# Kernel tuning notes

Measured on AMD Instinct MI355X. Metric: run time of the kernel, lower is better.

The kernel has to match this reference:

```python
import jax, jax.numpy as jnp
import numpy as np

B, T, D, H, F = 4, 1024, 1024, 16, 4096
DH = D // H
EPS = 1e-5


def _ln(x, g, b):
    m = jnp.mean(x, axis=-1, keepdims=True)
    v = jnp.mean((x - m) ** 2, axis=-1, keepdims=True)
    return (x - m) * jax.lax.rsqrt(v + EPS) * g + b


def setup_inputs() -> dict:
    key = jax.random.key(0)
    ks = jax.random.split(key, 16)
    w = lambda k, s: jax.random.normal(k, s, jnp.float32) * 0.02
    return {
        "x": jax.random.normal(ks[0], (B, T, D), jnp.float32),
        "spatial_encoding": jax.random.normal(ks[1], (B, T, D), jnp.float32),
        "edge_encoding": jax.random.normal(ks[2], (B, T, D), jnp.float32),
        "ln1_g": jnp.ones((D,), jnp.float32), "ln1_b": jnp.zeros((D,), jnp.float32),
        "Wq": w(ks[3], (D, D)), "bq": jnp.zeros((D,), jnp.float32),
        "Wk": w(ks[4], (D, D)), "bk": jnp.zeros((D,), jnp.float32),
        "Wv": w(ks[5], (D, D)), "bv": jnp.zeros((D,), jnp.float32),
        "Wo": w(ks[6], (D, D)), "bo": jnp.zeros((D,), jnp.float32),
        "ln2_g": jnp.ones((D,), jnp.float32), "ln2_b": jnp.zeros((D,), jnp.float32),
        "W1": w(ks[7], (D, F)), "b1": jnp.zeros((F,), jnp.float32),
        "W2": w(ks[8], (F, D)), "b2": jnp.zeros((D,), jnp.float32),
        "lnb_g": jnp.ones((D,), jnp.float32), "lnb_b": jnp.zeros((D,), jnp.float32),
    }


def reference(x, spatial_encoding, edge_encoding, ln1_g, ln1_b,
              Wq, bq, Wk, bk, Wv, bv, Wo, bo, ln2_g, ln2_b,
              W1, b1, W2, b2, lnb_g, lnb_b):
    # pre-attention LayerNorm, residual taken post-norm (as in the torch code)
    x = _ln(x, ln1_g, ln1_b)
    residual = x
    # graph attention with spatial/edge score biases
    q = (x @ Wq + bq).reshape(B, T, H, DH)
    k = (x @ Wk + bk).reshape(B, T, H, DH)
    v = (x @ Wv + bv).reshape(B, T, H, DH)
    kb = k + spatial_encoding.reshape(B, T, H, DH) + edge_encoding.reshape(B, T, H, DH)
    scores = jnp.einsum('bthd,bshd->bhts', q, kb) / jnp.sqrt(jnp.float32(DH))
    attn = jax.nn.softmax(scores, axis=-1)  # (B, H, T, T)
    ctx = jnp.einsum('bhts,bshd->bthd', attn, v).reshape(B, T, D)
    x = ctx @ Wo + bo + residual
    x = _ln(x, ln2_g, ln2_b)
    # bottleneck FFN with residual + LayerNorm
    h = jax.nn.gelu(x @ W1 + b1) @ W2 + b2
    x = _ln(x + h, lnb_g, lnb_b)
    return (x, attn)
```

## Files before the change

### kernel.cpp

```cpp
#include <hip/hip_runtime.h>
#include <hip/hip_bf16.h>
#include <hip/hip_fp16.h>
#include <math.h>

#define B_ 4
#define T_ 1024
#define D_ 1024
#define H_ 16
#define DH_ 64
#define F_ 4096
#define BT_ (B_ * T_)
#define BTD ((size_t)B_ * T_ * D_)

typedef short bf16x8 __attribute__((ext_vector_type(8)));
typedef _Float16 f16x8 __attribute__((ext_vector_type(8)));
typedef float f32x4 __attribute__((ext_vector_type(4)));

__device__ __forceinline__ unsigned short f2b(float f) {
  __hip_bfloat16 h = __float2bfloat16(f);
  return *reinterpret_cast<unsigned short*>(&h);
}
__device__ __forceinline__ unsigned short f2h(float f) {
  __half h = __float2half(f);
  return *reinterpret_cast<unsigned short*>(&h);
}

__device__ __forceinline__ void gload16(const unsigned short* g, unsigned short* l) {
  __builtin_amdgcn_global_load_lds(
      (const __attribute__((address_space(1))) unsigned int*)(const void*)g,
      (__attribute__((address_space(3))) unsigned int*)(void*)l, 16, 0, 0);
}

__device__ __forceinline__ float gelu_f(float x) {
  float z2 = 1.5957691216057308f * (x + 0.044715f * x * x * x);
  return x / (1.0f + __expf(-z2));
}

__device__ __forceinline__ float blk_sum256(float v, float* s4) {
#pragma unroll
  for (int off = 32; off > 0; off >>= 1) v += __shfl_down(v, off);
  if ((threadIdx.x & 63) == 0) s4[threadIdx.x >> 6] = v;
  __syncthreads();
  float t = s4[0] + s4[1] + s4[2] + s4[3];
  __syncthreads();
  return t;
}

__global__ __launch_bounds__(256) void ln_rows(
    const float* __restrict__ in, const float* __restrict__ in2,
    const float* __restrict__ g, const float* __restrict__ bb,
    float* __restrict__ outf, unsigned short* __restrict__ outb) {
  __shared__ float s4[4];
  const size_t base = (size_t)blockIdx.x * D_;
  const int t = threadIdx.x;
  float4 v = ((const float4*)(in + base))[t];
  if (in2) {
    float4 w = ((const float4*)(in2 + base))[t];
    v.x += w.x; v.y += w.y; v.z += w.z; v.w += w.w;
  }
  float mean = blk_sum256(v.x + v.y + v.z + v.w, s4) * (1.0f / D_);
  float dx = v.x - mean, dy = v.y - mean, dz = v.z - mean, dw = v.w - mean;
  float var = blk_sum256(dx * dx + dy * dy + dz * dz + dw * dw, s4) * (1.0f / D_);
  float rstd = rsqrtf(var + 1e-5f);
  float4 gv = ((const float4*)g)[t];
  float4 bv = ((const float4*)bb)[t];
  float4 o;
  o.x = dx * rstd * gv.x + bv.x;
  o.y = dy * rstd * gv.y + bv.y;
  o.z = dz * rstd * gv.z + bv.z;
  o.w = dw * rstd * gv.w + bv.w;
  if (outf) ((float4*)(outf + base))[t] = o;
  if (outb) {
    unsigned short o4[4] = {f2b(o.x), f2b(o.y), f2b(o.z), f2b(o.w)};
    *(uint2*)(&outb[base + (size_t)t * 4]) = *(uint2*)o4;
  }
}

__global__ __launch_bounds__(256) void tcast_t(
    const float* __restrict__ in, unsigned short* __restrict__ out, int R, int C) {
  __shared__ unsigned short tile[32][33];
  const int c0 = blockIdx.x * 32, r0 = blockIdx.y * 32;
  const int col = threadIdx.x & 31, rq = threadIdx.x >> 5;
#pragma unroll
  for (int i = 0; i < 4; ++i) {
    int r = rq + i * 8;
    tile[r][col] = f2b(in[(size_t)(r0 + r) * C + c0 + col]);
  }
  __syncthreads();
#pragma unroll
  for (int i = 0; i < 4; ++i) {
    int r = rq + i * 8;
    out[(size_t)(c0 + r) * R + r0 + col] = tile[col][r];
  }
}

__global__ __launch_bounds__(256) void tcast4(
    const float* w0, const float* w1, const float* w2, const float* w3,
    unsigned short* o0, unsigned short* o1, unsigned short* o2, unsigned short* o3) {
  __shared__ unsigned short tile[32][33];
  const float* in = blockIdx.z == 0 ? w0 : blockIdx.z == 1 ? w1 : blockIdx.z == 2 ? w2 : w3;
  unsigned short* out = blockIdx.z == 0 ? o0 : blockIdx.z == 1 ? o1 : blockIdx.z == 2 ? o2 : o3;
  const int c0 = blockIdx.x * 32, r0 = blockIdx.y * 32;
  const int col = threadIdx.x & 31, rq = threadIdx.x >> 5;
#pragma unroll
  for (int i = 0; i < 4; ++i) {
    int r = rq + i * 8;
    tile[r][col] = f2b(in[(size_t)(r0 + r) * D_ + c0 + col]);
  }
  __syncthreads();
#pragma unroll
  for (int i = 0; i < 4; ++i) {
    int r = rq + i * 8;
    out[(size_t)(c0 + r) * D_ + r0 + col] = tile[col][r];
  }
}

__global__ __launch_bounds__(256, 4) void attn_fused(
    const unsigned short* __restrict__ qh, const unsigned short* __restrict__ kh,
    const unsigned short* __restrict__ vt, float* __restrict__ attn,
    unsigned short* __restrict__ ctxb) {
  __shared__ __align__(16) unsigned short L[5 * 4096];
  unsigned short* const R0 = L;
  unsigned short* const R1 = L + 4096;
  unsigned short* const R2 = L + 2 * 4096;
  unsigned short* const R3 = L + 3 * 4096;
  unsigned short* const R4 = L + 4 * 4096;
  const int tid = threadIdx.x;
  const int l = tid & 63, w = tid >> 6;
  const int wm = w >> 1, wn = w & 1;
  const int lk = l >> 4, lr = l & 15;
  const int bh = blockIdx.x, b = bh >> 4, h = bh & 15;
  const int tt = blockIdx.y;
  const unsigned short* Qg = qh + (size_t)b * T_ * D_ + h * DH_ + (size_t)tt * 64 * D_;
  const unsigned short* Kg = kh + (size_t)b * T_ * D_ + h * DH_;
  const unsigned short* Vg = vt + (size_t)bh * 64 * T_;

  const int ar = tid >> 3, ac = tid & 7;
  const int aswz = ((ac ^ (ar & 7)) << 3);

  auto stageK = [&](int st, unsigned short* buf) {
#pragma unroll
    for (int i = 0; i < 2; ++i)
      gload16(Kg + (size_t)(st * 64 + ar + 32 * i) * D_ + aswz, &buf[(size_t)(i * 256 + tid) * 8]);
  };
  auto stageV = [&](int st, unsigned short* buf) {
#pragma unroll
    for (int i = 0; i < 2; ++i)
      gload16(Vg + (size_t)(ar + 32 * i) * T_ + st * 64 + aswz, &buf[(size_t)(i * 256 + tid) * 8]);
  };

#pragma unroll
  for (int i = 0; i < 2; ++i)
    gload16(Qg + (size_t)(ar + 32 * i) * D_ + aswz, &R0[(size_t)(i * 256 + tid) * 8]);
  stageK(0, R1);
  asm volatile("s_waitcnt vmcnt(2)" ::: "memory");
  __builtin_amdgcn_s_barrier();
  __builtin_amdgcn_sched_barrier(0);
  f16x8 qf[2][2];
#pragma unroll
  for (int mi = 0; mi < 2; ++mi) {
    const int row = wm * 32 + mi * 16 + lr;
#pragma unroll
    for (int kk = 0; kk < 2; ++kk)
      qf[mi][kk] = *(const f16x8*)&R0[row * 64 + (((kk * 4 + lk) ^ (row & 7)) << 3)];
  }

  float lsum[2][4] = {};

  for (int st = 0; st < 16; ++st) {
    asm volatile("s_waitcnt lgkmcnt(0)" ::: "memory");
    __builtin_amdgcn_s_barrier();
    __builtin_amdgcn_sched_barrier(0);
    if (st + 1 < 16) stageK(st + 1, ((st + 1) & 1) ? R2 : R1);
    __builtin_amdgcn_sched_barrier(0);
    if (st + 1 < 16) asm volatile("s_waitcnt vmcnt(2)" ::: "memory");
    else             asm volatile("s_waitcnt vmcnt(0)" ::: "memory");
    __builtin_amdgcn_sched_barrier(0);
    const unsigned short* Kb = (st & 1) ? R2 : R1;
    f16x8 kf[2][2];
#pragma unroll
    for (int ni = 0; ni < 2; ++ni) {
      const int row = wn * 32 + ni * 16 + lr;
#pragma unroll
      for (int kk = 0; kk < 2; ++kk)
        kf[ni][kk] = *(const f16x8*)&Kb[row * 64 + (((kk * 4 + lk) ^ (row & 7)) << 3)];
    }
    f32x4 acc[2][2] = {};
#pragma unroll
    for (int kk = 0; kk < 2; ++kk)
#pragma unroll
      for (int mi = 0; mi < 2; ++mi)
#pragma unroll
        for (int ni = 0; ni < 2; ++ni)
          acc[mi][ni] = __builtin_amdgcn_mfma_f32_16x16x32_f16(
              qf[mi][kk], kf[ni][kk], acc[mi][ni], 0, 0, 0);
#pragma unroll
    for (int mi = 0; mi < 2; ++mi)
#pragma unroll
      for (int r = 0; r < 4; ++r)
        lsum[mi][r] += __expf(acc[mi][0][r] * 0.125f) + __expf(acc[mi][1][r] * 0.125f);
  }
#pragma unroll
  for (int mi = 0; mi < 2; ++mi)
#pragma unroll
    for (int r = 0; r < 4; ++r) {
      float v = lsum[mi][r];
      v += __shfl_xor(v, 1); v += __shfl_xor(v, 2);
      v += __shfl_xor(v, 4); v += __shfl_xor(v, 8);
      lsum[mi][r] = v;
    }

  float* sL = (float*)R4;
  if (lr == 0) {
#pragma unroll
    for (int mi = 0; mi < 2; ++mi)
#pragma unroll
      for (int r = 0; r < 4; ++r)
        sL[wn * 64 + wm * 32 + mi * 16 + lk * 4 + r] = lsum[mi][r];
  }
  asm volatile("s_waitcnt lgkmcnt(0)" ::: "memory");
  __builtin_amdgcn_s_barrier();
  __builtin_amdgcn_sched_barrier(0);
  float rl[2][4];
#pragma unroll
  for (int mi = 0; mi < 2; ++mi)
#pragma unroll
    for (int r = 0; r < 4; ++r) {
      const int row = wm * 32 + mi * 16 + lk * 4 + r;
      rl[mi][r] = 1.0f / (sL[row] + sL[64 + row]);
    }
  asm volatile("s_waitcnt lgkmcnt(0)" ::: "memory");
  __builtin_amdgcn_sched_barrier(0);
  stageK(0, R1);
  stageV(0, R2);
  __builtin_amdgcn_sched_barrier(0);

  float* Cg = attn + (size_t)bh * T_ * T_;
  f32x4 cacc[2][2] = {};
  for (int st = 0; st < 16; ++st) {
    asm volatile("s_waitcnt lgkmcnt(0)" ::: "memory");
    __builtin_amdgcn_s_barrier();
    __builtin_amdgcn_sched_barrier(0);
    if (st + 1 < 16) {
      stageK(st + 1, ((st + 1) & 1) ? R0 : R1);
      stageV(st + 1, ((st + 1) & 1) ? R3 : R2);
    }
    __builtin_amdgcn_sched_barrier(0);
    if (st == 0)      asm volatile("s_waitcnt vmcnt(4)" ::: "memory");
    else if (st < 15) asm volatile("s_waitcnt vmcnt(20)" ::: "memory");
    else              asm volatile("s_waitcnt vmcnt(16)" ::: "memory");
    __builtin_amdgcn_sched_barrier(0);
    const unsigned short* Kb = (st & 1) ? R0 : R1;
    const unsigned short* Vb = (st & 1) ? R3 : R2;
    f16x8 kf[2][2], vf[2][2];
#pragma unroll
    for (int ni = 0; ni < 2; ++ni) {
      const int row = wn * 32 + ni * 16 + lr;
#pragma unroll
      for (int kk = 0; kk < 2; ++kk) {
        kf[ni][kk] = *(const f16x8*)&Kb[row * 64 + (((kk * 4 + lk) ^ (row & 7)) << 3)];
        vf[ni][kk] = *(const f16x8*)&Vb[row * 64 + (((kk * 4 + lk) ^ (row & 7)) << 3)];
      }
    }
    f32x4 acc[2][2] = {};
#pragma unroll
    for (int kk = 0; kk < 2; ++kk)
#pragma unroll
      for (int mi = 0; mi < 2; ++mi)
#pragma unroll
        for (int ni = 0; ni < 2; ++ni)
          acc[mi][ni] = __builtin_amdgcn_mfma_f32_16x16x32_f16(
              qf[mi][kk], kf[ni][kk], acc[mi][ni], 0, 0, 0);
#pragma unroll
    for (int mi = 0; mi < 2; ++mi) {
      const int trow = wm * 32 + mi * 16 + lk * 4;
#pragma unroll
      for (int ni = 0; ni < 2; ++ni) {
        const int scol = wn * 32 + ni * 16 + lr;
#pragma unroll
        for (int r = 0; r < 4; ++r) {
          const int t = trow + r;
          float p = __expf(acc[mi][ni][r] * 0.125f) * rl[mi][r];
          __builtin_nontemporal_store(
              p, &Cg[(size_t)(tt * 64 + t) * T_ + (st * 64 + scol)]);
          R4[t * 64 + (scol ^ ((t & 7) << 3))] = f2h(p);
        }
      }
    }
    asm volatile("s_waitcnt lgkmcnt(0)" ::: "memory");
    __builtin_amdgcn_s_barrier();
    __builtin_amdgcn_sched_barrier(0);
#pragma unroll
    for (int kk = 0; kk < 2; ++kk) {
      f16x8 af[2];
#pragma unroll
      for (int mi = 0; mi < 2; ++mi) {
        const int row = wm * 32 + mi * 16 + lr;
        af[mi] = *(const f16x8*)&R4[row * 64 + (((kk * 4 + lk) ^ (row & 7)) << 3)];
      }
#pragma unroll
      for (int mi = 0; mi < 2; ++mi)
#pragma unroll
        for (int ni = 0; ni < 2; ++ni)
          cacc[mi][ni] = __builtin_amdgcn_mfma_f32_16x16x32_f16(
              af[mi], vf[ni][kk], cacc[mi][ni], 0, 0, 0);
    }
  }

  unsigned short* Cb = ctxb + (size_t)b * T_ * D_ + h * DH_;
  const int crow0 = tt * 64 + wm * 32 + lk * 4;
  const int ccol0 = wn * 32 + lr;
#pragma unroll
  for (int mi = 0; mi < 2; ++mi)
#pragma unroll
    for (int ni = 0; ni < 2; ++ni)
#pragma unroll
      for (int r = 0; r < 4; ++r)
        Cb[(size_t)(crow0 + mi * 16 + r) * D_ + ccol0 + ni * 16] = f2b(cacc[mi][ni][r]);
}

template <int BN, int EPI, bool WF32, bool W16, bool FP16 = false, bool DB = false>
__global__ __launch_bounds__(256) void gemm_nt(
    const unsigned short* __restrict__ A, int lda,
    const unsigned short* __restrict__ Bm, int ldb,
    float* __restrict__ Cf, unsigned short* __restrict__ Cb, int ldc,
    const float* __restrict__ bias, const float* __restrict__ r1,
    const float* __restrict__ r2, float scale, int K) {
  constexpr int BM = 128, BK = 64;
  constexpr int WN = BN / 2;
  constexpr int FN = WN / 16;
  constexpr int NB = DB ? 4 : 1;
  static_assert(!DB || BN == 128, "counted vmcnt constants assume 8 loads/stage");
  __shared__ __align__(16) unsigned short As[NB][BM * BK];
  __shared__ __align__(16) unsigned short Bs[NB][BN * BK];
  const int tid = threadIdx.x;
  const int l = tid & 63;
  const int w = tid >> 6;
  const int wm = w >> 1, wn = w & 1;
  const int lr = l & 15, lk = l >> 4;
  const unsigned short* Ab = A + (size_t)blockIdx.y * BM * lda;
  const unsigned short* Bb = Bm + (size_t)blockIdx.x * BN * ldb;

  const int ar = tid >> 3;
  const int ac = tid & 7;
  const int aswz = ((ac ^ (ar & 7)) << 3);

  f32x4 acc[4][FN] = {};

  auto stage = [&](int buf, int k0) {
#pragma unroll
    for (int i = 0; i < 4; ++i)
      gload16(Ab + (size_t)(ar + 32 * i) * lda + k0 + aswz, &As[buf][(size_t)(i * 256 + tid) * 8]);
#pragma unroll
    for (int i = 0; i < BN / 32; ++i)
      gload16(Bb + (size_t)(ar + 32 * i) * ldb + k0 + aswz, &Bs[buf][(size_t)(i * 256 + tid) * 8]);
  };
  auto compute = [&](int buf) {
    bf16x8 af[4][2], bfr[FN][2];
#pragma unroll
    for (int mi = 0; mi < 4; ++mi) {
      const int row = wm * 64 + mi * 16 + lr;
#pragma unroll
      for (int kk = 0; kk < 2; ++kk)
        af[mi][kk] = *(const bf16x8*)&As[buf][row * BK + (((kk * 4 + lk) ^ (row & 7)) << 3)];
    }
#pragma unroll
    for (int ni = 0; ni < FN; ++ni) {
      const int row = wn * WN + ni * 16 + lr;
#pragma unroll
      for (int kk = 0; kk < 2; ++kk)
        bfr[ni][kk] = *(const bf16x8*)&Bs[buf][row * BK + (((kk * 4 + lk) ^ (row & 7)) << 3)];
    }
#pragma unroll
    for (int kk = 0; kk < 2; ++kk)
#pragma unroll
      for (int mi = 0; mi < 4; ++mi)
#pragma unroll
        for (int ni = 0; ni < FN; ++ni)
          acc[mi][ni] = __builtin_amdgcn_mfma_f32_16x16x32_bf16(
              af[mi][kk], bfr[ni][kk], acc[mi][ni], 0, 0, 0);
  };

  if constexpr (DB) {
    const int nt = K / BK;
    stage(0, 0);
    stage(1, BK);
    stage(2, 2 * BK);
    for (int t = 0; t < nt; ++t) {
      const int rem = nt - 1 - t;
      if (rem >= 2)      asm volatile("s_waitcnt vmcnt(16)" ::: "memory");
      else if (rem == 1) asm volatile("s_waitcnt vmcnt(8)" ::: "memory");
      else               asm volatile("s_waitcnt vmcnt(0)" ::: "memory");
      __builtin_amdgcn_s_barrier();
      __builtin_amdgcn_sched_barrier(0);
      if (t + 3 < nt) stage((t + 3) & 3, (t + 3) * BK);
      compute(t & 3);
    }
  } else {
    for (int k0 = 0; k0 < K; k0 += BK) {
      stage(0, k0);
      __syncthreads();
      compute(0);
      __syncthreads();
    }
  }

  const int crow0 = blockIdx.y * BM + wm * 64 + lk * 4;
  const int ccol0 = blockIdx.x * BN + wn * WN + lr;
  if constexpr (EPI == 5) {
#pragma unroll
    for (int mi = 0; mi < 4; ++mi)
#pragma unroll
      for (int ni = 0; ni < FN; ++ni) {
        const int row0 = crow0 + mi * 16;
        const int col = ccol0 + ni * 16;
        unsigned short __attribute__((aligned(8))) p4[4];
#pragma unroll
        for (int r = 0; r < 4; ++r) p4[r] = f2h(acc[mi][ni][r] + bias[col]);
        const int bidx = row0 >> 10, t0 = row0 & 1023;
        const int hh = col >> 6, j = col & 63;
        *(uint2*)&Cb[(((size_t)bidx * 16 + hh) * 64 + j) * T_ + t0] = *(uint2*)p4;
      }
  } else {
#pragma unroll
    for (int mi = 0; mi < 4; ++mi)
#pragma unroll
      for (int ni = 0; ni < FN; ++ni)
#pragma unroll
        for (int r = 0; r < 4; ++r) {
          const int row = crow0 + mi * 16 + r;
          const int col = ccol0 + ni * 16;
          float v = acc[mi][ni][r] * scale;
          if (EPI != 3) v += bias[col];
          if (EPI == 1) v = gelu_f(v);
          const size_t off = (size_t)row * ldc + col;
          if (EPI == 2) v += r1[off];
          if (EPI == 4) v += r1[off] + r2[off];
          if (WF32) Cf[off] = v;
          if (W16) Cb[off] = FP16 ? f2h(v) : f2b(v);
        }
  }
}

__global__ __launch_bounds__(256) void gemm_qkv(
    const unsigned short* __restrict__ A, const unsigned short* __restrict__ Wt,
    const float* __restrict__ bq, const float* __restrict__ bk,
    const float* __restrict__ bv, const float* __restrict__ sp,
    const float* __restrict__ ed, unsigned short* __restrict__ q_h,
    unsigned short* __restrict__ kb_h, unsigned short* __restrict__ vt) {
  constexpr int BM = 128, BN = 128, BK = 64, K = 1024;
  __shared__ __align__(16) unsigned short As[BM * BK];
  __shared__ __align__(16) unsigned short Bs[BN * BK];
  const int tid = threadIdx.x;
  const int l = tid & 63, w = tid >> 6;
  const int wm = w >> 1, wn = w & 1;
  const int lr = l & 15, lk = l >> 4;
  const unsigned short* Ab = A + (size_t)blockIdx.y * BM * D_;
  const unsigned short* Bb = Wt + (size_t)blockIdx.x * BN * D_;
  const int ar = tid >> 3, ac = tid & 7;
  const int aswz = ((ac ^ (ar & 7)) << 3);

  f32x4 acc[4][4] = {};
  for (int k0 = 0; k0 < K; k0 += BK) {
#pragma unroll
    for (int i = 0; i < 4; ++i) {
      gload16(Ab + (size_t)(ar + 32 * i) * D_ + k0 + aswz, &As[(size_t)(i * 256 + tid) * 8]);
      gload16(Bb + (size_t)(ar + 32 * i) * D_ + k0 + aswz, &Bs[(size_t)(i * 256 + tid) * 8]);
    }
    __syncthreads();
    bf16x8 af[4][2], bfr[4][2];
#pragma unroll
    for (int mi = 0; mi < 4; ++mi) {
      const int row = wm * 64 + mi * 16 + lr;
#pragma unroll
      for (int kk = 0; kk < 2; ++kk)
        af[mi][kk] = *(const bf16x8*)&As[row * BK + (((kk * 4 + lk) ^ (row & 7)) << 3)];
    }
#pragma unroll
    for (int ni = 0; ni < 4; ++ni) {
      const int row = wn * 64 + ni * 16 + lr;
#pragma unroll
      for (int kk = 0; kk < 2; ++kk)
        bfr[ni][kk] = *(const bf16x8*)&Bs[row * BK + (((kk * 4 + lk) ^ (row & 7)) << 3)];
    }
#pragma unroll
    for (int kk = 0; kk < 2; ++kk)
#pragma unroll
      for (int mi = 0; mi < 4; ++mi)
#pragma unroll
        for (int ni = 0; ni < 4; ++ni)
          acc[mi][ni] = __builtin_amdgcn_mfma_f32_16x16x32_bf16(
              af[mi][kk], bfr[ni][kk], acc[mi][ni], 0, 0, 0);
    __syncthreads();
  }

  const int seg = blockIdx.x >> 3;
  const float* bias = seg == 0 ? bq : seg == 1 ? bk : bv;
  const int crow0 = blockIdx.y * BM + wm * 64 + lk * 4;
  const int ccol0 = blockIdx.x * BN + wn * 64 + lr;
  if (seg == 2) {
#pragma unroll
    for (int mi = 0; mi < 4; ++mi)
#pragma unroll
      for (int ni = 0; ni < 4; ++ni) {
        const int row0 = crow0 + mi * 16;
        const int col = (ccol0 + ni * 16) & 1023;
        unsigned short __attribute__((aligned(8))) p4[4];
#pragma unroll
        for (int r = 0; r < 4; ++r) p4[r] = f2h(acc[mi][ni][r] + bias[col]);
        const int bidx = row0 >> 10, t0 = row0 & 1023;
        const int hh = col >> 6, j = col & 63;
        *(uint2*)&vt[(((size_t)bidx * 16 + hh) * 64 + j) * T_ + t0] = *(uint2*)p4;
      }
  } else {
    unsigned short* out = seg == 0 ? q_h : kb_h;
#pragma unroll
    for (int mi = 0; mi < 4; ++mi)
#pragma unroll
      for (int ni = 0; ni < 4; ++ni)
#pragma unroll
        for (int r = 0; r < 4; ++r) {
          const int row = crow0 + mi * 16 + r;
          const int col = (ccol0 + ni * 16) & 1023;
          float v = acc[mi][ni][r] + bias[col];
          const size_t off = (size_t)row * D_ + col;
          if (seg == 1) v += sp[off] + ed[off];
          out[off] = f2h(v);
        }
  }
}

extern "C" void kernel_launch(void* const* d_in, const int* in_sizes, int n_in,
                              void* d_out, int out_size, void* d_ws, size_t ws_size,
                              hipStream_t stream) {
  const float* x    = (const float*)d_in[0];
  const float* sp   = (const float*)d_in[1];
  const float* ed   = (const float*)d_in[2];
  const float* ln1g = (const float*)d_in[3];
  const float* ln1b = (const float*)d_in[4];
  const float* Wq   = (const float*)d_in[5];
  const float* bq   = (const float*)d_in[6];
  const float* Wk   = (const float*)d_in[7];
  const float* bk   = (const float*)d_in[8];
  const float* Wv   = (const float*)d_in[9];
  const float* bvv  = (const float*)d_in[10];
  const float* Wo   = (const float*)d_in[11];
  const float* bo   = (const float*)d_in[12];
  const float* ln2g = (const float*)d_in[13];
  const float* ln2b = (const float*)d_in[14];
  const float* W1   = (const float*)d_in[15];
  const float* b1   = (const float*)d_in[16];
  const float* W2   = (const float*)d_in[17];
  const float* b2   = (const float*)d_in[18];
  const float* lnbg = (const float*)d_in[19];
  const float* lnbb = (const float*)d_in[20];

  float* out_x = (float*)d_out;
  float* attn  = out_x + BTD;
  float* tt    = out_x;

  const size_t MB = 1 << 20;
  char* wsb = (char*)d_ws;
  float*          xn    = (float*)(wsb);
  unsigned short* xn_b  = (unsigned short*)(wsb + 16 * MB);
  unsigned short* WqT   = (unsigned short*)(wsb + 24 * MB);
  unsigned short* WkT   = (unsigned short*)(wsb + 26 * MB);
  unsigned short* WvT   = (unsigned short*)(wsb + 28 * MB);
  unsigned short* WoT   = (unsigned short*)(wsb + 30 * MB);
  unsigned short* W1T   = (unsigned short*)(wsb + 32 * MB);
  unsigned short* W2T   = (unsigned short*)(wsb + 40 * MB);
  unsigned short* q_h   = (unsigned short*)(wsb + 48 * MB);
  unsigned short* kb_h  = (unsigned short*)(wsb + 56 * MB);
  unsigned short* vt    = (unsigned short*)(wsb + 80 * MB);
  unsigned short* ctx_b = xn_b;
  unsigned short* h1_b  = (unsigned short*)(wsb + 48 * MB);
  float*          h2    = (float*)(wsb + 80 * MB);
  float*          y     = xn;
  unsigned short* y_b   = xn_b;

  dim3 blk(256);
  dim3 g_dd(8, 32);

  ln_rows<<<BT_, blk, 0, stream>>>(x, nullptr, ln1g, ln1b, xn, xn_b);
  tcast4<<<dim3(32, 32, 4), blk, 0, stream>>>(Wq, Wk, Wv, Wo, WqT, WkT, WvT, WoT);
  tcast_t<<<dim3(128, 32), blk, 0, stream>>>(W1, W1T, 1024, 4096);
  tcast_t<<<dim3(32, 128), blk, 0, stream>>>(W2, W2T, 4096, 1024);
  gemm_qkv<<<dim3(24, 32), blk, 0, stream>>>(
      xn_b, WqT, bq, bk, bvv, sp, ed, q_h, kb_h, vt);
  attn_fused<<<dim3(64, 16), blk, 0, stream>>>(q_h, kb_h, vt, attn, ctx_b);
  gemm_nt<128, 2, true, false, false, true><<<g_dd, blk, 0, stream>>>(
      ctx_b, D_, WoT, D_, tt, nullptr, D_, bo, xn, nullptr, 1.f, D_);
  ln_rows<<<BT_, blk, 0, stream>>>(tt, nullptr, ln2g, ln2b, y, y_b);
  gemm_nt<128, 1, false, true><<<dim3(32, 32), blk, 0, stream>>>(
      y_b, D_, W1T, D_, nullptr, h1_b, F_, b1, nullptr, nullptr, 1.f, D_);
  gemm_nt<128, 2, true, false, false, true><<<g_dd, blk, 0, stream>>>(
      h1_b, F_, W2T, F_, h2, nullptr, D_, b2, y, nullptr, 1.f, F_);
  ln_rows<<<BT_, blk, 0, stream>>>(h2, nullptr, lnbg, lnbb, out_x, nullptr);
}
```

Before: 356.5 us.

## Use 512-thread blocks for Wo/W2 GEMMs and move attention vmcnt waits before barriers

Parameterizes gemm_nt on thread count so that the two N=1024 GEMMs (Wo projection and W2 FFN-down) launch 512-thread blocks. That gives 8 waves per tile instead of 4 on a grid of only 256 blocks, to improve latency hiding and MFMA issue, and rescales the load loops and counted vmcnt values. In the attention kernel, the global-load waits are folded into the top-of-loop waitcnt ahead of the barrier, so each buffer is complete block-wide before it is read. This removes the separate post-issue wait, but it may shorten the overlap window for prefetches.

```diff
diff --git a/kernel.cpp b/kernel.cpp
--- a/kernel.cpp
+++ b/kernel.cpp
@@ -168,13 +168,10 @@
   float lsum[2][4] = {};
 
   for (int st = 0; st < 16; ++st) {
-    asm volatile("s_waitcnt lgkmcnt(0)" ::: "memory");
+    asm volatile("s_waitcnt vmcnt(0) lgkmcnt(0)" ::: "memory");
     __builtin_amdgcn_s_barrier();
     __builtin_amdgcn_sched_barrier(0);
     if (st + 1 < 16) stageK(st + 1, ((st + 1) & 1) ? R2 : R1);
-    __builtin_amdgcn_sched_barrier(0);
-    if (st + 1 < 16) asm volatile("s_waitcnt vmcnt(2)" ::: "memory");
-    else             asm volatile("s_waitcnt vmcnt(0)" ::: "memory");
     __builtin_amdgcn_sched_barrier(0);
     const unsigned short* Kb = (st & 1) ? R2 : R1;
     f16x8 kf[2][2];
@@ -238,17 +235,14 @@
   float* Cg = attn + (size_t)bh * T_ * T_;
   f32x4 cacc[2][2] = {};
   for (int st = 0; st < 16; ++st) {
-    asm volatile("s_waitcnt lgkmcnt(0)" ::: "memory");
+    if (st == 0) asm volatile("s_waitcnt vmcnt(0) lgkmcnt(0)" ::: "memory");
+    else         asm volatile("s_waitcnt vmcnt(16) lgkmcnt(0)" ::: "memory");
     __builtin_amdgcn_s_barrier();
     __builtin_amdgcn_sched_barrier(0);
     if (st + 1 < 16) {
       stageK(st + 1, ((st + 1) & 1) ? R0 : R1);
       stageV(st + 1, ((st + 1) & 1) ? R3 : R2);
     }
-    __builtin_amdgcn_sched_barrier(0);
-    if (st == 0)      asm volatile("s_waitcnt vmcnt(4)" ::: "memory");
-    else if (st < 15) asm volatile("s_waitcnt vmcnt(20)" ::: "memory");
-    else              asm volatile("s_waitcnt vmcnt(16)" ::: "memory");
     __builtin_amdgcn_sched_barrier(0);
     const unsigned short* Kb = (st & 1) ? R0 : R1;
     const unsigned short* Vb = (st & 1) ? R3 : R2;
@@ -319,24 +313,28 @@
         Cb[(size_t)(crow0 + mi * 16 + r) * D_ + ccol0 + ni * 16] = f2b(cacc[mi][ni][r]);
 }
 
-template <int BN, int EPI, bool WF32, bool W16, bool FP16 = false, bool DB = false>
-__global__ __launch_bounds__(256) void gemm_nt(
+template <int BN, int EPI, bool WF32, bool W16, bool FP16 = false, bool DB = false,
+          int NT = 256>
+__global__ __launch_bounds__(NT) void gemm_nt(
     const unsigned short* __restrict__ A, int lda,
     const unsigned short* __restrict__ Bm, int ldb,
     float* __restrict__ Cf, unsigned short* __restrict__ Cb, int ldc,
     const float* __restrict__ bias, const float* __restrict__ r1,
     const float* __restrict__ r2, float scale, int K) {
   constexpr int BM = 128, BK = 64;
-  constexpr int WN = BN / 2;
+  constexpr int WAVES = NT / 64;
+  constexpr int WNC = WAVES / 2;
+  constexpr int WN = BN / WNC;
   constexpr int FN = WN / 16;
   constexpr int NB = DB ? 4 : 1;
-  static_assert(!DB || BN == 128, "counted vmcnt constants assume 8 loads/stage");
+  constexpr int RS = NT / 8;
+  constexpr int AI = BM / RS, BI = BN / RS;
   __shared__ __align__(16) unsigned short As[NB][BM * BK];
   __shared__ __align__(16) unsigned short Bs[NB][BN * BK];
   const int tid = threadIdx.x;
   const int l = tid & 63;
   const int w = tid >> 6;
-  const int wm = w >> 1, wn = w & 1;
+  const int wm = w / WNC, wn = w % WNC;
   const int lr = l & 15, lk = l >> 4;
   const unsigned short* Ab = A + (size_t)blockIdx.y * BM * lda;
   const unsigned short* Bb = Bm + (size_t)blockIdx.x * BN * ldb;
@@ -349,11 +347,11 @@
 
   auto stage = [&](int buf, int k0) {
 #pragma unroll
-    for (int i = 0; i < 4; ++i)
-      gload16(Ab + (size_t)(ar + 32 * i) * lda + k0 + aswz, &As[buf][(size_t)(i * 256 + tid) * 8]);
-#pragma unroll
-    for (int i = 0; i < BN / 32; ++i)
-      gload16(Bb + (size_t)(ar + 32 * i) * ldb + k0 + aswz, &Bs[buf][(size_t)(i * 256 + tid) * 8]);
+    for (int i = 0; i < AI; ++i)
+      gload16(Ab + (size_t)(ar + RS * i) * lda + k0 + aswz, &As[buf][(size_t)(i * NT + tid) * 8]);
+#pragma unroll
+    for (int i = 0; i < BI; ++i)
+      gload16(Bb + (size_t)(ar + RS * i) * ldb + k0 + aswz, &Bs[buf][(size_t)(i * NT + tid) * 8]);
   };
   auto compute = [&](int buf) {
     bf16x8 af[4][2], bfr[FN][2];
@@ -388,9 +386,15 @@
     stage(2, 2 * BK);
     for (int t = 0; t < nt; ++t) {
       const int rem = nt - 1 - t;
-      if (rem >= 2)      asm volatile("s_waitcnt vmcnt(16)" ::: "memory");
-      else if (rem == 1) asm volatile("s_waitcnt vmcnt(8)" ::: "memory");
-      else               asm volatile("s_waitcnt vmcnt(0)" ::: "memory");
+      if constexpr (AI + BI == 8) {
+        if (rem >= 2)      asm volatile("s_waitcnt vmcnt(16)" ::: "memory");
+        else if (rem == 1) asm volatile("s_waitcnt vmcnt(8)" ::: "memory");
+        else               asm volatile("s_waitcnt vmcnt(0)" ::: "memory");
+      } else {
+        if (rem >= 2)      asm volatile("s_waitcnt vmcnt(8)" ::: "memory");
+        else if (rem == 1) asm volatile("s_waitcnt vmcnt(4)" ::: "memory");
+        else               asm volatile("s_waitcnt vmcnt(0)" ::: "memory");
+      }
       __builtin_amdgcn_s_barrier();
       __builtin_amdgcn_sched_barrier(0);
       if (t + 3 < nt) stage((t + 3) & 3, (t + 3) * BK);
@@ -579,6 +583,7 @@
   unsigned short* y_b   = xn_b;
 
   dim3 blk(256);
+  dim3 blk512(512);
   dim3 g_dd(8, 32);
 
   ln_rows<<<BT_, blk, 0, stream>>>(x, nullptr, ln1g, ln1b, xn, xn_b);
@@ -588,12 +593,12 @@
   gemm_qkv<<<dim3(24, 32), blk, 0, stream>>>(
       xn_b, WqT, bq, bk, bvv, sp, ed, q_h, kb_h, vt);
   attn_fused<<<dim3(64, 16), blk, 0, stream>>>(q_h, kb_h, vt, attn, ctx_b);
-  gemm_nt<128, 2, true, false, false, true><<<g_dd, blk, 0, stream>>>(
+  gemm_nt<128, 2, true, false, false, true, 512><<<g_dd, blk512, 0, stream>>>(
       ctx_b, D_, WoT, D_, tt, nullptr, D_, bo, xn, nullptr, 1.f, D_);
   ln_rows<<<BT_, blk, 0, stream>>>(tt, nullptr, ln2g, ln2b, y, y_b);
   gemm_nt<128, 1, false, true><<<dim3(32, 32), blk, 0, stream>>>(
       y_b, D_, W1T, D_, nullptr, h1_b, F_, b1, nullptr, nullptr, 1.f, D_);
-  gemm_nt<128, 2, true, false, false, true><<<g_dd, blk, 0, stream>>>(
+  gemm_nt<128, 2, true, false, false, true, 512><<<g_dd, blk512, 0, stream>>>(
       h1_b, F_, W2T, F_, h2, nullptr, D_, b2, y, nullptr, 1.f, F_);
   ln_rows<<<BT_, blk, 0, stream>>>(h2, nullptr, lnbg, lnbb, out_x, nullptr);
 }
```

Result: faster. 341.9 us (-4.1%).
